# Optimization experiments

Measured on AMD Instinct MI355X. Metric: run time of the kernel, lower is better.

The kernel has to match this reference:

```python
import jax, jax.numpy as jnp
import numpy as np

VOCAB, E, H, OUT = 128, 768, 768, 768
B, T = 128, 512


def setup_inputs() -> dict:
    key = jax.random.key(0)
    ks = jax.random.split(key, 8)
    s_emb = 1.0  # torch nn.Embedding default init is N(0,1)
    s_gru = 1.0 / np.sqrt(H)  # torch GRU init U(-1/sqrt(H), 1/sqrt(H))
    s_fc = 1.0 / np.sqrt(H)
    return {
        "x": jax.random.randint(ks[0], (B, T), 0, VOCAB),
        "emb": jax.random.normal(ks[1], (VOCAB, E), dtype=jnp.float32) * s_emb,
        "W_ih": jax.random.uniform(ks[2], (3 * H, E), jnp.float32, -s_gru, s_gru),
        "W_hh": jax.random.uniform(ks[3], (3 * H, H), jnp.float32, -s_gru, s_gru),
        "b_ih": jax.random.uniform(ks[4], (3 * H,), jnp.float32, -s_gru, s_gru),
        "b_hh": jax.random.uniform(ks[5], (3 * H,), jnp.float32, -s_gru, s_gru),
        "fc_W": jax.random.uniform(ks[6], (OUT, H), jnp.float32, -s_fc, s_fc),
        "fc_b": jax.random.uniform(ks[7], (OUT,), jnp.float32, -s_fc, s_fc),
    }


def _gru_last_hidden(xe, W_ih, W_hh, b_ih, b_hh):
    # xe: [B, T, E]. Precompute all input-side gate pre-activations in one GEMM.
    gx = jnp.einsum("bte,ge->btg", xe, W_ih) + b_ih  # [B, T, 3H]
    gx = jnp.swapaxes(gx, 0, 1)  # [T, B, 3H] for scan
    h0 = jnp.zeros((xe.shape[0], W_hh.shape[1]), xe.dtype)

    def step(h, gx_t):
        gh = h @ W_hh.T + b_hh  # [B, 3H]
        xr, xz, xn = jnp.split(gx_t, 3, axis=-1)
        hr, hz, hn = jnp.split(gh, 3, axis=-1)
        r = jax.nn.sigmoid(xr + hr)
        z = jax.nn.sigmoid(xz + hz)
        n = jnp.tanh(xn + r * hn)
        h_new = (1.0 - z) * n + z * h
        return h_new, None

    h_last, _ = jax.lax.scan(step, h0, gx)
    return h_last  # [B, H]


def reference(x, emb, W_ih, W_hh, b_ih, b_hh, fc_W, fc_b):
    xe = jnp.take(emb, x, axis=0)  # [B, T, E]
    h = _gru_last_hidden(xe, W_ih, W_hh, b_ih, b_hh)
    return h @ fc_W.T + fc_b  # [B, OUT]
```

## Files before the change

kernel.cpp:

```cpp
#include <hip/hip_runtime.h>

#define DI __device__ __forceinline__

constexpr int BB   = 128;
constexpr int TT   = 512;
constexpr int HH   = 768;
constexpr int G3   = 3 * HH;
constexpr int VOC  = 128;

constexpr int NU   = 48;
constexpr int UB   = 16;
constexpr int NGRP = 4;
constexpr int BGRP = 32;
constexpr int KC   = 24;

constexpr size_t OFF_GE    = 0;
constexpr size_t OFF_WIMG  = 1179648;
constexpr size_t OFF_H16   = OFF_WIMG + 3538944;
constexpr size_t OFF_H32   = OFF_H16 + 393216;
constexpr size_t OFF_FLAGS = OFF_H32 + 393216;

constexpr int LDS_W_BYTES = 73728;
constexpr int LDS_BYTES   = 90112;

typedef _Float16 f16x8 __attribute__((ext_vector_type(8)));
typedef float    f32x4 __attribute__((ext_vector_type(4)));

DI float sigm(float x) { return __builtin_amdgcn_rcpf(1.0f + __expf(-x)); }
DI float tanh_fast(float x) {
  float e = __expf(-2.0f * fabsf(x));
  float r = (1.0f - e) * __builtin_amdgcn_rcpf(1.0f + e);
  return copysignf(r, x);
}

DI f16x8 load_l3_x4(const void* p) {
  f16x8 r;
  asm volatile("global_load_dwordx4 %0, %1, off sc0 sc1"
               : "=v"(r) : "v"(p) : "memory");
  return r;
}
DI void store_l3_x2(void* p, uint2 v) {
  asm volatile("global_store_dwordx2 %0, %1, off sc0 sc1"
               :: "v"(p), "v"(v) : "memory");
}
DI void wait_vm0() { asm volatile("s_waitcnt vmcnt(0)" ::: "memory"); }
DI void wait_lgkm0() { asm volatile("s_waitcnt lgkmcnt(0)" ::: "memory"); }

__global__ void k_zero(uint4* h16q, int n16, int* flags, int nflags) {
  int i = blockIdx.x * 256 + threadIdx.x;
  uint4 z; z.x = 0; z.y = 0; z.z = 0; z.w = 0;
  if (i < n16) h16q[i] = z;
  if (i < nflags) flags[i] = 0;
}

__global__ void k_prep_w(const float* __restrict__ Whh, _Float16* __restrict__ wimg) {
  int tid = blockIdx.x * 256 + threadIdx.x;
  if (tid >= NU * 3 * KC * 64) return;
  int l  = tid & 63;
  int fi = tid >> 6;
  int kc = fi % KC;
  int nt = (fi / KC) % 3;
  int j  = fi / (KC * 3);
  int g  = nt * HH + j * UB + (l & 15);
  int k0 = kc * 32 + (l >> 4) * 8;
  const float* src = Whh + (size_t)g * HH + k0;
  f16x8 o;
#pragma unroll
  for (int q = 0; q < 8; ++q) o[q] = (_Float16)src[q];
  ((f16x8*)wimg)[tid] = o;
}

__global__ void k_prep_ge(const float* __restrict__ emb, const float* __restrict__ Wih,
                          const float* __restrict__ bih, float* __restrict__ ge) {
  int g  = blockIdx.x * 256 + threadIdx.x;
  int v0 = blockIdx.y * 16;
  float acc[16];
  float b = bih[g];
#pragma unroll
  for (int i = 0; i < 16; ++i) acc[i] = b;
  const float* wrow = Wih + (size_t)g * HH;
  for (int e = 0; e < HH; e += 4) {
    float4 w = *(const float4*)(wrow + e);
#pragma unroll
    for (int i = 0; i < 16; ++i) {
      float4 m = *(const float4*)(emb + (size_t)(v0 + i) * HH + e);
      acc[i] = fmaf(w.x, m.x, acc[i]);
      acc[i] = fmaf(w.y, m.y, acc[i]);
      acc[i] = fmaf(w.z, m.z, acc[i]);
      acc[i] = fmaf(w.w, m.w, acc[i]);
    }
  }
#pragma unroll
  for (int i = 0; i < 16; ++i) ge[(size_t)(v0 + i) * G3 + g] = acc[i];
}

__global__ __launch_bounds__(128, 1) void k_gru(
    const int* __restrict__ x,
    const float* __restrict__ ge,
    const float* __restrict__ bhh,
    const _Float16* __restrict__ wimg,
    _Float16* h16,
    float* __restrict__ h32,
    int* flags)
{
  extern __shared__ char smem[];
  _Float16* lds = (_Float16*)smem;
  _Float16* st  = (_Float16*)(smem + LDS_W_BYTES);

  const int tid  = threadIdx.x;
  const int lane = tid & 63;
  const int wid  = tid >> 6;
  const int bid  = blockIdx.x;
  const int grp  = bid / NU;
  const int j    = bid % NU;
  const int b0   = grp * BGRP;
  const int u0   = j * UB;
  int* gflags = flags + grp * NU;

  {
    const uint4* src = (const uint4*)(wimg + (size_t)j * (3 * KC * 64 * 8));
    uint4* dst = (uint4*)lds;
#pragma unroll
    for (int r = 0; r < 36; ++r) dst[tid + 128 * r] = src[tid + 128 * r];
  }

  const int col  = lane & 15;
  const int krow = lane >> 4;
  const int bm   = b0 + wid * 16;

  const float bh_r = bhh[0 * HH + u0 + col];
  const float bh_z = bhh[1 * HH + u0 + col];
  const float bh_n = bhh[2 * HH + u0 + col];

  float hprev[4] = {0.f, 0.f, 0.f, 0.f};

  _Float16* hb0 = h16;
  _Float16* hb1 = h16 + (size_t)BB * HH;

  __syncthreads();

  for (int t = 0; t < TT; ++t) {
    int xv[4];
#pragma unroll
    for (int q = 0; q < 4; ++q) xv[q] = x[(size_t)(bm + krow * 4 + q) * TT + t];
    float ger[4], gez[4], gen[4];
#pragma unroll
    for (int q = 0; q < 4; ++q) {
      const float* gp = ge + (size_t)xv[q] * G3 + u0 + col;
      ger[q] = gp[0 * HH];
      gez[q] = gp[1 * HH];
      gen[q] = gp[2 * HH];
    }

    if (t > 0) {
      const bool act = lane < NU;
      for (;;) {
        int f = act ? __hip_atomic_load(&gflags[lane], __ATOMIC_RELAXED,
                                        __HIP_MEMORY_SCOPE_AGENT)
                    : t;
        if (__all(f >= t)) break;
        __builtin_amdgcn_s_sleep(1);
      }
    }
    asm volatile("" ::: "memory");

    const _Float16* hb = (t & 1) ? hb1 : hb0;
    const char* abase = (const char*)(hb + (size_t)(bm + col) * HH + krow * 8);
    f16x8 a[KC];
#pragma unroll
    for (int kc = 0; kc < KC; ++kc) a[kc] = load_l3_x4(abase + kc * 64);
    wait_vm0();
    __builtin_amdgcn_sched_barrier(0);

    f32x4 acc0 = {bh_r, bh_r, bh_r, bh_r};
    f32x4 acc1 = {bh_z, bh_z, bh_z, bh_z};
    f32x4 acc2 = {bh_n, bh_n, bh_n, bh_n};
    const f16x8* bfr = (const f16x8*)lds;
#pragma unroll
    for (int kc = 0; kc < KC; ++kc) {
      acc0 = __builtin_amdgcn_mfma_f32_16x16x32_f16(a[kc], bfr[(0 * KC + kc) * 64 + lane], acc0, 0, 0, 0);
      acc1 = __builtin_amdgcn_mfma_f32_16x16x32_f16(a[kc], bfr[(1 * KC + kc) * 64 + lane], acc1, 0, 0, 0);
      acc2 = __builtin_amdgcn_mfma_f32_16x16x32_f16(a[kc], bfr[(2 * KC + kc) * 64 + lane], acc2, 0, 0, 0);
    }

    float hv[4];
#pragma unroll
    for (int q = 0; q < 4; ++q) {
      float r = sigm(acc0[q] + ger[q]);
      float z = sigm(acc1[q] + gez[q]);
      float n = tanh_fast(gen[q] + r * acc2[q]);
      float h = n + z * (hprev[q] - n);
      hprev[q] = h;
      hv[q] = h;
    }

    if (t == TT - 1) {
#pragma unroll
      for (int q = 0; q < 4; ++q)
        h32[(size_t)(bm + krow * 4 + q) * HH + u0 + col] = hv[q];
    } else {
#pragma unroll
      for (int q = 0; q < 4; ++q)
        st[wid * 256 + (krow * 4 + q) * 16 + col] = (_Float16)hv[q];
      wait_lgkm0();
      __builtin_amdgcn_sched_barrier(0);
      int rr = lane >> 2;
      int qq = lane & 3;
      uint2 v = *(const uint2*)&st[wid * 256 + rr * 16 + qq * 4];
      _Float16* hn = (t & 1) ? hb0 : hb1;
      store_l3_x2((char*)(hn + (size_t)(bm + rr) * HH + u0 + qq * 4), v);
      wait_vm0();
      __syncthreads();
      if (tid == 0)
        __hip_atomic_store(&gflags[j], t + 1, __ATOMIC_RELAXED,
                           __HIP_MEMORY_SCOPE_AGENT);
    }
  }
}

__global__ void k_fc(const float* __restrict__ h32, const float* __restrict__ fcW,
                     const float* __restrict__ fcb, float* __restrict__ out) {
  int o  = blockIdx.x * 256 + threadIdx.x;
  int b0 = blockIdx.y * 16;
  float acc[16];
  float bi = fcb[o];
#pragma unroll
  for (int i = 0; i < 16; ++i) acc[i] = bi;
  const float* wrow = fcW + (size_t)o * HH;
  for (int e = 0; e < HH; e += 4) {
    float4 w = *(const float4*)(wrow + e);
#pragma unroll
    for (int i = 0; i < 16; ++i) {
      float4 m = *(const float4*)(h32 + (size_t)(b0 + i) * HH + e);
      acc[i] = fmaf(w.x, m.x, acc[i]);
      acc[i] = fmaf(w.y, m.y, acc[i]);
      acc[i] = fmaf(w.z, m.z, acc[i]);
      acc[i] = fmaf(w.w, m.w, acc[i]);
    }
  }
#pragma unroll
  for (int i = 0; i < 16; ++i) out[(size_t)(b0 + i) * HH + o] = acc[i];
}

extern "C" void kernel_launch(void* const* d_in, const int* in_sizes, int n_in,
                              void* d_out, int out_size, void* d_ws, size_t ws_size,
                              hipStream_t stream) {
  const int*   x   = (const int*)d_in[0];
  const float* emb = (const float*)d_in[1];
  const float* Wih = (const float*)d_in[2];
  const float* Whh = (const float*)d_in[3];
  const float* bih = (const float*)d_in[4];
  const float* bhh = (const float*)d_in[5];
  const float* fcW = (const float*)d_in[6];
  const float* fcb = (const float*)d_in[7];
  float* out = (float*)d_out;

  char* ws = (char*)d_ws;
  float*     ge    = (float*)(ws + OFF_GE);
  _Float16*  wimg  = (_Float16*)(ws + OFF_WIMG);
  _Float16*  h16   = (_Float16*)(ws + OFF_H16);
  float*     h32   = (float*)(ws + OFF_H32);
  int*       flags = (int*)(ws + OFF_FLAGS);

  k_zero<<<96, 256, 0, stream>>>((uint4*)h16, 24576, flags, NGRP * NU);
  k_prep_w<<<864, 256, 0, stream>>>(Whh, wimg);
  k_prep_ge<<<dim3(9, 8), 256, 0, stream>>>(emb, Wih, bih, ge);

  hipFuncSetAttribute(reinterpret_cast<const void*>(k_gru),
                      hipFuncAttributeMaxDynamicSharedMemorySize, LDS_BYTES);
  k_gru<<<NGRP * NU, 128, LDS_BYTES, stream>>>(x, ge, bhh, wimg, h16, h32, flags);

  k_fc<<<dim3(3, 8), 256, 0, stream>>>(h32, fcW, fcb, out);
}
```

Before: 2.740 ms.

## Keep W_hh in registers, use per-wave flags, prefetch next-step gate inputs

The recurrent weight fragments now live in VGPRs for the whole kernel instead of being read from LDS at every step. The block-level __syncthreads before flag publication is replaced by one flag per wave, and consumers poll both flags with a single 64-bit load and no sleep. The next timestep's token and input-gate values are loaded while the h store is in flight, and the staging buffer is padded to avoid LDS bank conflicts. Holding 72 f16x8 fragments per lane raises register pressure considerably and may cause spills, and busy-polling without sleep adds memory traffic.

```diff
diff --git a/kernel.cpp b/kernel.cpp
--- a/kernel.cpp
+++ b/kernel.cpp
@@ -20,8 +20,7 @@
 constexpr size_t OFF_H32   = OFF_H16 + 393216;
 constexpr size_t OFF_FLAGS = OFF_H32 + 393216;
 
-constexpr int LDS_W_BYTES = 73728;
-constexpr int LDS_BYTES   = 90112;
+constexpr int LDS_BYTES = 90112;
 
 typedef _Float16 f16x8 __attribute__((ext_vector_type(8)));
 typedef float    f32x4 __attribute__((ext_vector_type(4)));
@@ -104,8 +103,7 @@
     int* flags)
 {
   extern __shared__ char smem[];
-  _Float16* lds = (_Float16*)smem;
-  _Float16* st  = (_Float16*)(smem + LDS_W_BYTES);
+  _Float16* st = (_Float16*)smem;
 
   const int tid  = threadIdx.x;
   const int lane = tid & 63;
@@ -115,19 +113,22 @@
   const int j    = bid % NU;
   const int b0   = grp * BGRP;
   const int u0   = j * UB;
-  int* gflags = flags + grp * NU;
-
-  {
-    const uint4* src = (const uint4*)(wimg + (size_t)j * (3 * KC * 64 * 8));
-    uint4* dst = (uint4*)lds;
-#pragma unroll
-    for (int r = 0; r < 36; ++r) dst[tid + 128 * r] = src[tid + 128 * r];
-  }
+  int* gflags = flags + grp * NU * 2;
 
   const int col  = lane & 15;
   const int krow = lane >> 4;
   const int bm   = b0 + wid * 16;
 
+  f16x8 bfr[3][KC];
+  {
+    const f16x8* wsrc = (const f16x8*)wimg + (size_t)j * (3 * KC * 64) + lane;
+#pragma unroll
+    for (int nt = 0; nt < 3; ++nt)
+#pragma unroll
+      for (int kc = 0; kc < KC; ++kc)
+        bfr[nt][kc] = wsrc[(nt * KC + kc) * 64];
+  }
+
   const float bh_r = bhh[0 * HH + u0 + col];
   const float bh_z = bhh[1 * HH + u0 + col];
   const float bh_n = bhh[2 * HH + u0 + col];
@@ -137,29 +138,31 @@
   _Float16* hb0 = h16;
   _Float16* hb1 = h16 + (size_t)BB * HH;
 
-  __syncthreads();
-
-  for (int t = 0; t < TT; ++t) {
-    int xv[4];
-#pragma unroll
-    for (int q = 0; q < 4; ++q) xv[q] = x[(size_t)(bm + krow * 4 + q) * TT + t];
-    float ger[4], gez[4], gen[4];
+  float ger[4], gez[4], gen[4];
+  {
 #pragma unroll
     for (int q = 0; q < 4; ++q) {
-      const float* gp = ge + (size_t)xv[q] * G3 + u0 + col;
+      int xv = x[(size_t)(bm + krow * 4 + q) * TT + 0];
+      const float* gp = ge + (size_t)xv * G3 + u0 + col;
       ger[q] = gp[0 * HH];
       gez[q] = gp[1 * HH];
       gen[q] = gp[2 * HH];
     }
-
+  }
+
+  for (int t = 0; t < TT; ++t) {
     if (t > 0) {
       const bool act = lane < NU;
+      const unsigned long long ok =
+          ((unsigned long long)(unsigned)t << 32) | (unsigned)t;
       for (;;) {
-        int f = act ? __hip_atomic_load(&gflags[lane], __ATOMIC_RELAXED,
-                                        __HIP_MEMORY_SCOPE_AGENT)
-                    : t;
-        if (__all(f >= t)) break;
-        __builtin_amdgcn_s_sleep(1);
+        unsigned long long f2 =
+            act ? __hip_atomic_load((const unsigned long long*)(gflags + lane * 2),
+                                    __ATOMIC_RELAXED, __HIP_MEMORY_SCOPE_AGENT)
+                : ok;
+        int lo = (int)(f2 & 0xffffffffu);
+        int hi = (int)(f2 >> 32);
+        if (__all(lo >= t && hi >= t)) break;
       }
     }
     asm volatile("" ::: "memory");
@@ -175,12 +178,11 @@
     f32x4 acc0 = {bh_r, bh_r, bh_r, bh_r};
     f32x4 acc1 = {bh_z, bh_z, bh_z, bh_z};
     f32x4 acc2 = {bh_n, bh_n, bh_n, bh_n};
-    const f16x8* bfr = (const f16x8*)lds;
 #pragma unroll
     for (int kc = 0; kc < KC; ++kc) {
-      acc0 = __builtin_amdgcn_mfma_f32_16x16x32_f16(a[kc], bfr[(0 * KC + kc) * 64 + lane], acc0, 0, 0, 0);
-      acc1 = __builtin_amdgcn_mfma_f32_16x16x32_f16(a[kc], bfr[(1 * KC + kc) * 64 + lane], acc1, 0, 0, 0);
-      acc2 = __builtin_amdgcn_mfma_f32_16x16x32_f16(a[kc], bfr[(2 * KC + kc) * 64 + lane], acc2, 0, 0, 0);
+      acc0 = __builtin_amdgcn_mfma_f32_16x16x32_f16(a[kc], bfr[0][kc], acc0, 0, 0, 0);
+      acc1 = __builtin_amdgcn_mfma_f32_16x16x32_f16(a[kc], bfr[1][kc], acc1, 0, 0, 0);
+      acc2 = __builtin_amdgcn_mfma_f32_16x16x32_f16(a[kc], bfr[2][kc], acc2, 0, 0, 0);
     }
 
     float hv[4];
@@ -201,18 +203,27 @@
     } else {
 #pragma unroll
       for (int q = 0; q < 4; ++q)
-        st[wid * 256 + (krow * 4 + q) * 16 + col] = (_Float16)hv[q];
+        st[wid * 320 + (krow * 4 + q) * 20 + col] = (_Float16)hv[q];
       wait_lgkm0();
       __builtin_amdgcn_sched_barrier(0);
       int rr = lane >> 2;
       int qq = lane & 3;
-      uint2 v = *(const uint2*)&st[wid * 256 + rr * 16 + qq * 4];
+      uint2 v = *(const uint2*)&st[wid * 320 + rr * 20 + qq * 4];
       _Float16* hn = (t & 1) ? hb0 : hb1;
       store_l3_x2((char*)(hn + (size_t)(bm + rr) * HH + u0 + qq * 4), v);
+
+#pragma unroll
+      for (int q = 0; q < 4; ++q) {
+        int xv = x[(size_t)(bm + krow * 4 + q) * TT + (t + 1)];
+        const float* gp = ge + (size_t)xv * G3 + u0 + col;
+        ger[q] = gp[0 * HH];
+        gez[q] = gp[1 * HH];
+        gen[q] = gp[2 * HH];
+      }
+
       wait_vm0();
-      __syncthreads();
-      if (tid == 0)
-        __hip_atomic_store(&gflags[j], t + 1, __ATOMIC_RELAXED,
+      if (lane == 0)
+        __hip_atomic_store(&gflags[j * 2 + wid], t + 1, __ATOMIC_RELAXED,
                            __HIP_MEMORY_SCOPE_AGENT);
     }
   }
@@ -262,7 +273,7 @@
   float*     h32   = (float*)(ws + OFF_H32);
   int*       flags = (int*)(ws + OFF_FLAGS);
 
-  k_zero<<<96, 256, 0, stream>>>((uint4*)h16, 24576, flags, NGRP * NU);
+  k_zero<<<96, 256, 0, stream>>>((uint4*)h16, 24576, flags, NGRP * NU * 2);
   k_prep_w<<<864, 256, 0, stream>>>(Whh, wimg);
   k_prep_ge<<<dim3(9, 8), 256, 0, stream>>>(emb, Wih, bih, ge);
 
```

Measured after the change: 3.108 ms. 13.4% more time.

## Split GRU into single-wave blocks with per-step atomic counters per batch group

Applied to the files above, without the earlier changes.

The persistent GRU kernel now runs 384 one-wave blocks (8 batch groups of 16 rows × 48 unit slices) instead of 192 two-wave blocks. Each block owns its own synchronisation domain. The per-block flag array polled by 48 lanes is replaced by a single per-timestep arrival counter that each block increments atomically, and waiters poll that one word. The next step's x/ge gather is prefetched before the flag signal, step 0 skips the matmul so h16 no longer needs zeroing, and the LDS staging uses a padded stride. Risks include more blocks contending on one counter, and a bounded spin budget that could break out early and read stale state.

```diff
diff --git a/kernel.cpp b/kernel.cpp
--- a/kernel.cpp
+++ b/kernel.cpp
@@ -4,24 +4,23 @@
 
 constexpr int BB   = 128;
 constexpr int TT   = 512;
+constexpr int TT1  = TT + 1;
 constexpr int HH   = 768;
 constexpr int G3   = 3 * HH;
 constexpr int VOC  = 128;
 
-constexpr int NU   = 48;
-constexpr int UB   = 16;
-constexpr int NGRP = 4;
-constexpr int BGRP = 32;
+constexpr int NG   = 8;
+constexpr int NW   = 48;
 constexpr int KC   = 24;
 
-constexpr size_t OFF_GE    = 0;
-constexpr size_t OFF_WIMG  = 1179648;
-constexpr size_t OFF_H16   = OFF_WIMG + 3538944;
-constexpr size_t OFF_H32   = OFF_H16 + 393216;
-constexpr size_t OFF_FLAGS = OFF_H32 + 393216;
-
-constexpr int LDS_W_BYTES = 73728;
-constexpr int LDS_BYTES   = 90112;
+constexpr size_t OFF_GE   = 0;
+constexpr size_t OFF_WIMG = 1179648;
+constexpr size_t OFF_H16  = OFF_WIMG + 3538944;
+constexpr size_t OFF_H32  = OFF_H16 + 393216;
+constexpr size_t OFF_CNT  = OFF_H32 + 393216;
+
+constexpr int LDS_W_BYTES = 3 * KC * 64 * 16;
+constexpr int LDS_BYTES   = LDS_W_BYTES + 1024;
 
 typedef _Float16 f16x8 __attribute__((ext_vector_type(8)));
 typedef float    f32x4 __attribute__((ext_vector_type(4)));
@@ -33,35 +32,39 @@
   return copysignf(r, x);
 }
 
-DI f16x8 load_l3_x4(const void* p) {
+DI f16x8 load_dc_x4(const void* p) {
   f16x8 r;
   asm volatile("global_load_dwordx4 %0, %1, off sc0 sc1"
                : "=v"(r) : "v"(p) : "memory");
   return r;
 }
-DI void store_l3_x2(void* p, uint2 v) {
+DI void store_dc_x2(void* p, uint2 v) {
   asm volatile("global_store_dwordx2 %0, %1, off sc0 sc1"
                :: "v"(p), "v"(v) : "memory");
 }
+DI int load_cnt(const int* p) {
+  int r;
+  asm volatile("global_load_dword %0, %1, off sc0 sc1\n\ts_waitcnt vmcnt(0)"
+               : "=v"(r) : "v"(p) : "memory");
+  return r;
+}
 DI void wait_vm0() { asm volatile("s_waitcnt vmcnt(0)" ::: "memory"); }
 DI void wait_lgkm0() { asm volatile("s_waitcnt lgkmcnt(0)" ::: "memory"); }
 
-__global__ void k_zero(uint4* h16q, int n16, int* flags, int nflags) {
+__global__ void k_zero(int* cnt, int n) {
   int i = blockIdx.x * 256 + threadIdx.x;
-  uint4 z; z.x = 0; z.y = 0; z.z = 0; z.w = 0;
-  if (i < n16) h16q[i] = z;
-  if (i < nflags) flags[i] = 0;
+  if (i < n) cnt[i] = 0;
 }
 
 __global__ void k_prep_w(const float* __restrict__ Whh, _Float16* __restrict__ wimg) {
   int tid = blockIdx.x * 256 + threadIdx.x;
-  if (tid >= NU * 3 * KC * 64) return;
+  if (tid >= NW * 3 * KC * 64) return;
   int l  = tid & 63;
   int fi = tid >> 6;
   int kc = fi % KC;
   int nt = (fi / KC) % 3;
   int j  = fi / (KC * 3);
-  int g  = nt * HH + j * UB + (l & 15);
+  int g  = nt * HH + j * 16 + (l & 15);
   int k0 = kc * 32 + (l >> 4) * 8;
   const float* src = Whh + (size_t)g * HH + k0;
   f16x8 o;
@@ -94,93 +97,87 @@
   for (int i = 0; i < 16; ++i) ge[(size_t)(v0 + i) * G3 + g] = acc[i];
 }
 
-__global__ __launch_bounds__(128, 1) void k_gru(
+__global__ __launch_bounds__(64, 1) void k_gru(
     const int* __restrict__ x,
     const float* __restrict__ ge,
     const float* __restrict__ bhh,
     const _Float16* __restrict__ wimg,
     _Float16* h16,
     float* __restrict__ h32,
-    int* flags)
+    int* cnt)
 {
   extern __shared__ char smem[];
-  _Float16* lds = (_Float16*)smem;
-  _Float16* st  = (_Float16*)(smem + LDS_W_BYTES);
-
-  const int tid  = threadIdx.x;
-  const int lane = tid & 63;
-  const int wid  = tid >> 6;
+  _Float16* st = (_Float16*)(smem + LDS_W_BYTES);
+
+  const int lane = threadIdx.x;
   const int bid  = blockIdx.x;
-  const int grp  = bid / NU;
-  const int j    = bid % NU;
-  const int b0   = grp * BGRP;
-  const int u0   = j * UB;
-  int* gflags = flags + grp * NU;
+  const int grp  = bid / NW;
+  const int j    = bid % NW;
+  const int bm   = grp * 16;
+  const int u0   = j * 16;
+  int* gcnt = cnt + grp * TT1;
 
   {
     const uint4* src = (const uint4*)(wimg + (size_t)j * (3 * KC * 64 * 8));
-    uint4* dst = (uint4*)lds;
-#pragma unroll
-    for (int r = 0; r < 36; ++r) dst[tid + 128 * r] = src[tid + 128 * r];
-  }
-
-  const int col  = lane & 15;
-  const int krow = lane >> 4;
-  const int bm   = b0 + wid * 16;
-
-  const float bh_r = bhh[0 * HH + u0 + col];
-  const float bh_z = bhh[1 * HH + u0 + col];
-  const float bh_n = bhh[2 * HH + u0 + col];
+    uint4* dst = (uint4*)smem;
+#pragma unroll 8
+    for (int r = 0; r < 72; ++r) dst[lane + 64 * r] = src[lane + 64 * r];
+  }
+
+  const int c16 = lane & 15;
+  const int kr  = lane >> 4;
+
+  const float bh_r = bhh[0 * HH + u0 + c16];
+  const float bh_z = bhh[1 * HH + u0 + c16];
+  const float bh_n = bhh[2 * HH + u0 + c16];
 
   float hprev[4] = {0.f, 0.f, 0.f, 0.f};
 
   _Float16* hb0 = h16;
   _Float16* hb1 = h16 + (size_t)BB * HH;
-
-  __syncthreads();
+  const f16x8* bfr = (const f16x8*)smem;
+
+  float ger[4], gez[4], gen[4];
+#pragma unroll
+  for (int q = 0; q < 4; ++q) {
+    int xv = x[(size_t)(bm + kr * 4 + q) * TT + 0];
+    const float* gp = ge + (size_t)xv * G3 + u0 + c16;
+    ger[q] = gp[0 * HH];
+    gez[q] = gp[1 * HH];
+    gen[q] = gp[2 * HH];
+  }
+
+  int budget = 1 << 20;
 
   for (int t = 0; t < TT; ++t) {
-    int xv[4];
-#pragma unroll
-    for (int q = 0; q < 4; ++q) xv[q] = x[(size_t)(bm + krow * 4 + q) * TT + t];
-    float ger[4], gez[4], gen[4];
-#pragma unroll
-    for (int q = 0; q < 4; ++q) {
-      const float* gp = ge + (size_t)xv[q] * G3 + u0 + col;
-      ger[q] = gp[0 * HH];
-      gez[q] = gp[1 * HH];
-      gen[q] = gp[2 * HH];
-    }
-
-    if (t > 0) {
-      const bool act = lane < NU;
-      for (;;) {
-        int f = act ? __hip_atomic_load(&gflags[lane], __ATOMIC_RELAXED,
-                                        __HIP_MEMORY_SCOPE_AGENT)
-                    : t;
-        if (__all(f >= t)) break;
-        __builtin_amdgcn_s_sleep(1);
-      }
-    }
-    asm volatile("" ::: "memory");
-
-    const _Float16* hb = (t & 1) ? hb1 : hb0;
-    const char* abase = (const char*)(hb + (size_t)(bm + col) * HH + krow * 8);
-    f16x8 a[KC];
-#pragma unroll
-    for (int kc = 0; kc < KC; ++kc) a[kc] = load_l3_x4(abase + kc * 64);
-    wait_vm0();
-    __builtin_amdgcn_sched_barrier(0);
-
     f32x4 acc0 = {bh_r, bh_r, bh_r, bh_r};
     f32x4 acc1 = {bh_z, bh_z, bh_z, bh_z};
     f32x4 acc2 = {bh_n, bh_n, bh_n, bh_n};
-    const f16x8* bfr = (const f16x8*)lds;
-#pragma unroll
-    for (int kc = 0; kc < KC; ++kc) {
-      acc0 = __builtin_amdgcn_mfma_f32_16x16x32_f16(a[kc], bfr[(0 * KC + kc) * 64 + lane], acc0, 0, 0, 0);
-      acc1 = __builtin_amdgcn_mfma_f32_16x16x32_f16(a[kc], bfr[(1 * KC + kc) * 64 + lane], acc1, 0, 0, 0);
-      acc2 = __builtin_amdgcn_mfma_f32_16x16x32_f16(a[kc], bfr[(2 * KC + kc) * 64 + lane], acc2, 0, 0, 0);
+
+    if (t > 0) {
+      const int* cp = gcnt + t;
+      for (;;) {
+        int c = load_cnt(cp);
+        if (c >= NW) break;
+        if (--budget < 0) break;
+        __builtin_amdgcn_s_sleep(1);
+      }
+      asm volatile("" ::: "memory");
+
+      const _Float16* hb = (t & 1) ? hb1 : hb0;
+      const char* ab = (const char*)(hb + (size_t)(bm + c16) * HH) + kr * 16;
+      f16x8 a[KC];
+#pragma unroll
+      for (int kc = 0; kc < KC; ++kc) a[kc] = load_dc_x4(ab + kc * 64);
+      wait_vm0();
+      __builtin_amdgcn_sched_barrier(0);
+
+#pragma unroll
+      for (int kc = 0; kc < KC; ++kc) {
+        acc0 = __builtin_amdgcn_mfma_f32_16x16x32_f16(a[kc], bfr[(0 * KC + kc) * 64 + lane], acc0, 0, 0, 0);
+        acc1 = __builtin_amdgcn_mfma_f32_16x16x32_f16(a[kc], bfr[(1 * KC + kc) * 64 + lane], acc1, 0, 0, 0);
+        acc2 = __builtin_amdgcn_mfma_f32_16x16x32_f16(a[kc], bfr[(2 * KC + kc) * 64 + lane], acc2, 0, 0, 0);
+      }
     }
 
     float hv[4];
@@ -197,23 +194,32 @@
     if (t == TT - 1) {
 #pragma unroll
       for (int q = 0; q < 4; ++q)
-        h32[(size_t)(bm + krow * 4 + q) * HH + u0 + col] = hv[q];
+        h32[(size_t)(bm + kr * 4 + q) * HH + u0 + c16] = hv[q];
     } else {
 #pragma unroll
       for (int q = 0; q < 4; ++q)
-        st[wid * 256 + (krow * 4 + q) * 16 + col] = (_Float16)hv[q];
+        st[(kr * 4 + q) * 20 + c16] = (_Float16)hv[q];
       wait_lgkm0();
       __builtin_amdgcn_sched_barrier(0);
       int rr = lane >> 2;
       int qq = lane & 3;
-      uint2 v = *(const uint2*)&st[wid * 256 + rr * 16 + qq * 4];
+      uint2 v = *(const uint2*)&st[rr * 20 + qq * 4];
       _Float16* hn = (t & 1) ? hb0 : hb1;
-      store_l3_x2((char*)(hn + (size_t)(bm + rr) * HH + u0 + qq * 4), v);
+      store_dc_x2((char*)(hn + (size_t)(bm + rr) * HH + u0 + qq * 4), v);
+
+#pragma unroll
+      for (int q = 0; q < 4; ++q) {
+        int xv = x[(size_t)(bm + kr * 4 + q) * TT + (t + 1)];
+        const float* gp = ge + (size_t)xv * G3 + u0 + c16;
+        ger[q] = gp[0 * HH];
+        gez[q] = gp[1 * HH];
+        gen[q] = gp[2 * HH];
+      }
+
       wait_vm0();
-      __syncthreads();
-      if (tid == 0)
-        __hip_atomic_store(&gflags[j], t + 1, __ATOMIC_RELAXED,
-                           __HIP_MEMORY_SCOPE_AGENT);
+      if (lane == 0)
+        __hip_atomic_fetch_add(gcnt + t + 1, 1, __ATOMIC_RELAXED,
+                               __HIP_MEMORY_SCOPE_AGENT);
     }
   }
 }
@@ -256,19 +262,19 @@
   float* out = (float*)d_out;
 
   char* ws = (char*)d_ws;
-  float*     ge    = (float*)(ws + OFF_GE);
-  _Float16*  wimg  = (_Float16*)(ws + OFF_WIMG);
-  _Float16*  h16   = (_Float16*)(ws + OFF_H16);
-  float*     h32   = (float*)(ws + OFF_H32);
-  int*       flags = (int*)(ws + OFF_FLAGS);
-
-  k_zero<<<96, 256, 0, stream>>>((uint4*)h16, 24576, flags, NGRP * NU);
+  float*     ge   = (float*)(ws + OFF_GE);
+  _Float16*  wimg = (_Float16*)(ws + OFF_WIMG);
+  _Float16*  h16  = (_Float16*)(ws + OFF_H16);
+  float*     h32  = (float*)(ws + OFF_H32);
+  int*       cnt  = (int*)(ws + OFF_CNT);
+
+  k_zero<<<17, 256, 0, stream>>>(cnt, NG * TT1);
   k_prep_w<<<864, 256, 0, stream>>>(Whh, wimg);
   k_prep_ge<<<dim3(9, 8), 256, 0, stream>>>(emb, Wih, bih, ge);
 
   hipFuncSetAttribute(reinterpret_cast<const void*>(k_gru),
                       hipFuncAttributeMaxDynamicSharedMemorySize, LDS_BYTES);
-  k_gru<<<NGRP * NU, 128, LDS_BYTES, stream>>>(x, ge, bhh, wimg, h16, h32, flags);
+  k_gru<<<NG * NW, 64, LDS_BYTES, stream>>>(x, ge, bhh, wimg, h16, h32, cnt);
 
   k_fc<<<dim3(3, 8), 256, 0, stream>>>(h32, fcW, fcb, out);
 }
```

Result: slower. 3.329 ms (+21.5%).
